# Kernel optimization log

Measured on AMD Instinct MI355X. Metric: run time of the kernel, lower is better.

Reference implementation:

```python
import jax, jax.numpy as jnp
import numpy as np

B, N, C, H = 4, 1024, 1024, 16
DH = C // H  # 64
EPS = 1e-5   # nn.LayerNorm default


def _layernorm(x, g, b):
    m = x.mean(-1, keepdims=True)
    v = ((x - m) ** 2).mean(-1, keepdims=True)
    return (x - m) * jax.lax.rsqrt(v + EPS) * g + b


def _rot_half(x):
    d = x.shape[-1] // 2
    return jnp.concatenate([-x[..., d:], x[..., :d]], axis=-1)


def _apply_rope_cat(x, emb):
    # emb: [N, 2*DH] = sin || cos (torch tensor_split(2, -1) order)
    sin, cos = jnp.split(emb, 2, axis=-1)  # each [N, DH]
    return x * cos + _rot_half(x) * sin


def setup_inputs() -> dict:
    key = jax.random.key(0)
    ks = jax.random.split(key, 12)
    s = 0.02
    x = jax.random.normal(ks[0], (B, N, C), jnp.float32)
    delta_t_emb = jax.random.normal(ks[1], (B, N, C), jnp.float32)
    v_residual_v1 = jax.random.normal(ks[2], (B, H, N, DH), jnp.float32)
    # realistic rope table: sin||cos, each DH wide (freqs repeated twice for rotate_half)
    pos = jnp.arange(N, dtype=jnp.float32)
    inv_freq = 1.0 / (10000.0 ** (jnp.arange(0, DH // 2, dtype=jnp.float32) / (DH // 2)))
    freqs = pos[:, None] * inv_freq[None, :]          # [N, DH/2]
    freqs = jnp.concatenate([freqs, freqs], axis=-1)  # [N, DH]
    rope = jnp.concatenate([jnp.sin(freqs), jnp.cos(freqs)], axis=-1)  # [N, 2*DH]
    Wqkv = jax.random.normal(ks[3], (3 * C, C), jnp.float32) * s
    bqkv = jnp.zeros((3 * C,), jnp.float32)
    Wdt = jax.random.normal(ks[4], (3 * C, C), jnp.float32) * s
    bdt = jnp.zeros((3 * C,), jnp.float32)
    qn_g = jnp.ones((DH,), jnp.float32); qn_b = jnp.zeros((DH,), jnp.float32)
    kn_g = jnp.ones((DH,), jnp.float32); kn_b = jnp.zeros((DH,), jnp.float32)
    lamb1 = jnp.asarray(0.5, jnp.float32)
    lamb2 = jnp.asarray(0.5, jnp.float32)
    Wproj = jax.random.normal(ks[5], (C, C), jnp.float32) * s
    bproj = jnp.zeros((C,), jnp.float32)
    return {
        "x": x, "rope": rope, "delta_t_emb": delta_t_emb, "v_residual_v1": v_residual_v1,
        "Wqkv": Wqkv, "bqkv": bqkv, "Wdt": Wdt, "bdt": bdt,
        "qn_g": qn_g, "qn_b": qn_b, "kn_g": kn_g, "kn_b": kn_b,
        "lamb1": lamb1, "lamb2": lamb2, "Wproj": Wproj, "bproj": bproj,
    }


def reference(x, rope, delta_t_emb, v_residual_v1, Wqkv, bqkv, Wdt, bdt,
              qn_g, qn_b, kn_g, kn_b, lamb1, lamb2, Wproj, bproj):
    b, n, c = x.shape
    # fused QKV: [B,N,3C] -> [3,B,H,N,DH]
    qkv = (jnp.einsum('bnc,oc->bno', x, Wqkv) + bqkv).reshape(b, n, 3, H, DH)
    qkv = jnp.transpose(qkv, (2, 0, 3, 1, 4))
    q, k, v = qkv[0], qkv[1], qkv[2]
    # delta-t additive embeddings
    dqkv = (jnp.einsum('bnc,oc->bno', delta_t_emb, Wdt) + bdt).reshape(b, n, 3, H, DH)
    dqkv = jnp.transpose(dqkv, (2, 0, 3, 1, 4))
    q = q + dqkv[0]; k = k + dqkv[1]; v = v + dqkv[2]
    # value-residual mixing
    v = lamb1 * v + lamb2 * v_residual_v1
    # qk layernorm over head_dim
    q = _layernorm(q, qn_g, qn_b)
    k = _layernorm(k, kn_g, kn_b)
    # RoPE (num_prefix_tokens = 0, rotate_half=True)
    q = _apply_rope_cat(q, rope)
    k = _apply_rope_cat(k, rope)
    # SDPA, non-causal, no dropout
    scale = 1.0 / jnp.sqrt(jnp.asarray(DH, x.dtype))
    scores = jnp.einsum('bhqd,bhkd->bhqk', q, k) * scale
    attn = jax.nn.softmax(scores, axis=-1)
    out = jnp.einsum('bhqk,bhkd->bhqd', attn, v)
    # [B,H,N,DH] -> [B,N,C], output norm is Identity (scale_norm=False)
    out = jnp.transpose(out, (0, 2, 1, 3)).reshape(b, n, c)
    out = jnp.einsum('bnc,oc->bno', out, Wproj) + bproj
    return out
```

## Files before the change

kernel.cpp:

```cpp
#include <hip/hip_runtime.h>
#include <stdint.h>

typedef unsigned short u16;
typedef __attribute__((ext_vector_type(8))) short short8;
typedef __attribute__((ext_vector_type(4))) float f32x4;
typedef __attribute__((ext_vector_type(4))) unsigned short u16x4;

#define DEVI __device__ __forceinline__

DEVI u16 f2bf(float f) {
  uint32_t u = __builtin_bit_cast(uint32_t, f);
  u += 0x7fffu + ((u >> 16) & 1u);
  return (u16)(u >> 16);
}

DEVI void gload_lds16(const void* g, void* l) {
  __builtin_amdgcn_global_load_lds(
      (const __attribute__((address_space(1))) void*)g,
      (__attribute__((address_space(3))) void*)(uint32_t)(uintptr_t)l,
      16, 0, 0);
}

__global__ void cvt_cat_bf16(const float* __restrict__ a, const float* __restrict__ b,
                             u16* __restrict__ dst, long total) {
  for (long i = ((long)blockIdx.x * 256 + threadIdx.x) * 4; i < total;
       i += (long)gridDim.x * 1024) {
    const long row = i >> 11;
    const long c = i & 2047;
    const float* src = (c < 1024) ? (a + row * 1024 + c) : (b + row * 1024 + (c - 1024));
    const float4 v = *(const float4*)src;
    u16x4 o = {f2bf(v.x), f2bf(v.y), f2bf(v.z), f2bf(v.w)};
    *(u16x4*)(dst + i) = o;
  }
}

__global__ void cvt_bf16(const float* __restrict__ a, u16* __restrict__ dst, long total) {
  for (long i = ((long)blockIdx.x * 256 + threadIdx.x) * 4; i < total;
       i += (long)gridDim.x * 1024) {
    const float4 v = *(const float4*)(a + i);
    u16x4 o = {f2bf(v.x), f2bf(v.y), f2bf(v.z), f2bf(v.w)};
    *(u16x4*)(dst + i) = o;
  }
}

__global__ __launch_bounds__(256, 2)
void gemm_bt(const u16* __restrict__ A, const u16* __restrict__ B,
             float* __restrict__ C, const float* __restrict__ bias1,
             const float* __restrict__ bias2, int M, int N, int K) {
  __shared__ u16 As[128 * 32];
  __shared__ u16 Bs[128 * 32];
  const int t = threadIdx.x;
  const int w = t >> 6, l = t & 63;
  const int l15 = l & 15, lg = l >> 4;
  const int bm = blockIdx.x, bn = blockIdx.y;
  const int wr = (w >> 1) * 64, wc = (w & 1) * 64;
  f32x4 acc[4][4] = {};
  const int c0 = w * 64 + l;

  for (int kt = 0; kt < (K >> 5); ++kt) {
#pragma unroll
    for (int i = 0; i < 2; ++i) {
      const int c = i * 256 + c0;
      const int row = c >> 2, seg = c & 3;
      gload_lds16(A + (long)(bm * 128 + row) * K + kt * 32 + seg * 8,
                  (char*)As + w * 1024 + i * 4096);
      gload_lds16(B + (long)(bn * 128 + row) * K + kt * 32 + seg * 8,
                  (char*)Bs + w * 1024 + i * 4096);
    }
    __syncthreads();
    short8 af[4], bfr[4];
#pragma unroll
    for (int m = 0; m < 4; ++m)
      af[m] = *(const short8*)&As[(wr + m * 16 + l15) * 32 + lg * 8];
#pragma unroll
    for (int n = 0; n < 4; ++n)
      bfr[n] = *(const short8*)&Bs[(wc + n * 16 + l15) * 32 + lg * 8];
#pragma unroll
    for (int m = 0; m < 4; ++m)
#pragma unroll
      for (int n = 0; n < 4; ++n)
        acc[m][n] = __builtin_amdgcn_mfma_f32_16x16x32_bf16(af[m], bfr[n], acc[m][n], 0, 0, 0);
    __syncthreads();
  }
#pragma unroll
  for (int m = 0; m < 4; ++m) {
    const int row0 = bm * 128 + wr + m * 16 + lg * 4;
#pragma unroll
    for (int n = 0; n < 4; ++n) {
      const int col = bn * 128 + wc + n * 16 + l15;
      float bia = 0.f;
      if (bias1) bia += bias1[col];
      if (bias2) bia += bias2[col];
#pragma unroll
      for (int r = 0; r < 4; ++r)
        C[(long)(row0 + r) * N + col] = acc[m][n][r] + bia;
    }
  }
}

__global__ __launch_bounds__(512, 2)
void gemm256(const u16* __restrict__ A, const u16* __restrict__ B,
             float* __restrict__ C, const float* __restrict__ bias1,
             const float* __restrict__ bias2, int M, int N, int K) {
  __shared__ u16 lds[4][16384];
  const int t = threadIdx.x;
  const int w = t >> 6, l = t & 63;
  const int l15 = l & 15, lg = l >> 4;
  const int wr = w >> 2, wc = w & 3;
  const int nbn = N >> 8;
  const int nb = gridDim.x;
  const int bid = blockIdx.x;
  const int lid = ((nb & 7) == 0) ? ((bid & 7) * (nb >> 3) + (bid >> 3)) : bid;
  const int bm = lid / nbn, bn = lid % nbn;
  const long rowA0 = (long)bm * 256;
  const long rowB0 = (long)bn * 256;
  const int nkt = K >> 5;

  const int su = (l & 7) ^ (l >> 3);
  const int rsub = 2 * (l >> 3) + (su >> 2);
  const int sg = su & 3;
  const int sfr = (lg + 4 * (l15 & 1)) ^ (l15 >> 1);

  f32x4 acc[8][4] = {};

#define STAGE(KT)                                                              \
  {                                                                            \
    const int _b = (KT) & 3;                                                   \
    _Pragma("unroll") for (int i = 0; i < 2; ++i) {                            \
      const int r = i * 128 + w * 16 + rsub;                                   \
      gload_lds16(A + (rowA0 + r) * K + (KT) * 32 + sg * 8,                    \
                  (char*)&lds[_b][(i * 64 + w * 8) * 64]);                     \
      gload_lds16(B + (rowB0 + r) * K + (KT) * 32 + sg * 8,                    \
                  (char*)&lds[_b][8192 + (i * 64 + w * 8) * 64]);              \
    }                                                                          \
  }

#define TILE(KT, VMSTR, DO_STAGE)                                              \
  {                                                                            \
    asm volatile("s_waitcnt vmcnt(" VMSTR ")" ::: "memory");                   \
    __builtin_amdgcn_s_barrier();                                              \
    asm volatile("" ::: "memory");                                             \
    __builtin_amdgcn_sched_barrier(0);                                         \
    if (DO_STAGE) STAGE((KT) + 3);                                             \
    const u16* bufp = lds[(KT) & 3];                                           \
    short8 bfr[4];                                                             \
    _Pragma("unroll") for (int n = 0; n < 4; ++n) {                            \
      const int p = wc * 32 + n * 8 + (l15 >> 1);                              \
      bfr[n] = *(const short8*)&bufp[8192 + p * 64 + sfr * 8];                 \
    }                                                                          \
    __builtin_amdgcn_s_setprio(1);                                             \
    _Pragma("unroll") for (int m = 0; m < 8; ++m) {                            \
      const int p = wr * 64 + m * 8 + (l15 >> 1);                              \
      const short8 af = *(const short8*)&bufp[p * 64 + sfr * 8];               \
      _Pragma("unroll") for (int n = 0; n < 4; ++n)                            \
        acc[m][n] = __builtin_amdgcn_mfma_f32_16x16x32_bf16(af, bfr[n],        \
                                                            acc[m][n], 0, 0, 0); \
    }                                                                          \
    __builtin_amdgcn_s_setprio(0);                                             \
  }

  STAGE(0)
  STAGE(1)
  STAGE(2)
  for (int kt = 0; kt < nkt - 2; ++kt) TILE(kt, "8", (kt + 3 < nkt))
  TILE(nkt - 2, "4", false)
  TILE(nkt - 1, "0", false)
#undef TILE
#undef STAGE

#pragma unroll
  for (int m = 0; m < 8; ++m) {
    const int row0 = bm * 256 + wr * 128 + m * 16 + lg * 4;
#pragma unroll
    for (int n = 0; n < 4; ++n) {
      const int col = bn * 256 + wc * 64 + n * 16 + l15;
      float bia = 0.f;
      if (bias1) bia += bias1[col];
      if (bias2) bia += bias2[col];
#pragma unroll
      for (int r = 0; r < 4; ++r)
        C[(long)(row0 + r) * N + col] = acc[m][n][r] + bia;
    }
  }
}

__global__ __launch_bounds__(256)
void fuse_qkv2(const float* __restrict__ qkv, const float* __restrict__ vres,
               const float* __restrict__ rope,
               const float* __restrict__ qg, const float* __restrict__ qb,
               const float* __restrict__ kg, const float* __restrict__ kb,
               const float* __restrict__ pl1, const float* __restrict__ pl2,
               u16* __restrict__ Q, u16* __restrict__ Ksw, u16* __restrict__ VTsw) {
  __shared__ u16 Vl[64][72];
  const int t = threadIdx.x, w = t >> 6, d = t & 63;
  const int bh = blockIdx.x, ntile = blockIdx.y;
  const int b = bh >> 4, h = bh & 15, n0 = ntile * 64;
  const float l1 = pl1[0], l2 = pl2[0];
  const float gq = qg[d], bq = qb[d];
  const float gk = kg[d], bk = kb[d];
  const float sgn = (d < 32) ? -1.f : 1.f;
  const int c = d >> 3, d7 = d & 7;

  for (int i = 0; i < 16; ++i) {
    const int nl = w * 16 + i;
    const int n = n0 + nl;
    const long base = ((long)(b * 1024 + n)) * 3072 + h * 64 + d;
    float q = qkv[base];
    float k = qkv[base + 1024];
    float v = qkv[base + 2048];
    v = l1 * v + l2 * vres[((long)(bh * 1024 + n)) * 64 + d];
    const float sinv = rope[n * 128 + d];
    const float cosv = rope[n * 128 + 64 + d];
    float s = q;
#pragma unroll
    for (int off = 1; off < 64; off <<= 1) s += __shfl_xor(s, off);
    const float qc = q - s * (1.f / 64.f);
    float vs = qc * qc;
#pragma unroll
    for (int off = 1; off < 64; off <<= 1) vs += __shfl_xor(vs, off);
    const float qn = qc * (1.f / sqrtf(vs * (1.f / 64.f) + 1e-5f)) * gq + bq;
    float s2 = k;
#pragma unroll
    for (int off = 1; off < 64; off <<= 1) s2 += __shfl_xor(s2, off);
    const float kc = k - s2 * (1.f / 64.f);
    float vs2 = kc * kc;
#pragma unroll
    for (int off = 1; off < 64; off <<= 1) vs2 += __shfl_xor(vs2, off);
    const float kn = kc * (1.f / sqrtf(vs2 * (1.f / 64.f) + 1e-5f)) * gk + bk;
    const float qo = __shfl_xor(qn, 32);
    const float ko = __shfl_xor(kn, 32);
    const float qr = qn * cosv + sgn * qo * sinv;
    const float kr = kn * cosv + sgn * ko * sinv;
    Q[(long)bh * 65536 + (long)n * 64 + d] = f2bf(qr);
    Ksw[(long)bh * 65536 + (long)n * 64 + ((c ^ (n & 7)) * 8 + d7)] = f2bf(kr);
    Vl[nl][d] = f2bf(v);
  }
  __syncthreads();
#pragma unroll
  for (int i = 0; i < 2; ++i) {
    const int task = i * 256 + t;
    const int dd = task >> 3, cc = task & 7;
    short8 o;
#pragma unroll
    for (int u = 0; u < 8; ++u) o[u] = (short)Vl[cc * 8 + u][dd];
    *(short8*)&VTsw[((long)(bh * 64 + dd)) * 1024 + n0 + ((cc ^ (dd & 7)) * 8)] = o;
  }
}

__global__ __launch_bounds__(256, 4)
void attn_fwd2(const u16* __restrict__ Q, const u16* __restrict__ Ksw,
               const u16* __restrict__ VTsw, u16* __restrict__ Out) {
  __shared__ u16 Kl[64 * 64];
  __shared__ u16 Vl[64 * 64];
  __shared__ u16 Pl[4][16 * 64];
  const int t = threadIdx.x, w = t >> 6, l = t & 63;
  const int l15 = l & 15, lg = l >> 4;
  const int x7 = l15 & 7;
  const int bh = blockIdx.x, q0 = blockIdx.y * 64;
  const long bo = (long)bh * 65536;
  u16* Plw = &Pl[w][0];

  const int qrow = q0 + w * 16 + l15;
  short8 qf[2];
#pragma unroll
  for (int ks = 0; ks < 2; ++ks)
    qf[ks] = *(const short8*)&Q[bo + (long)qrow * 64 + ks * 32 + lg * 8];

  f32x4 acc[4] = {};
  float m_run = -1e30f, l_run = 0.f;

  for (int kv = 0; kv < 16; ++kv) {
    const int kvb = kv * 64;
#pragma unroll
    for (int i = 0; i < 2; ++i) {
      const int idx = i * 256 + t;
      const int row = idx >> 3, seg = idx & 7;
      gload_lds16(Ksw + bo + (long)(kvb + row) * 64 + seg * 8, (char*)Kl + idx * 16);
      gload_lds16(VTsw + bo + (long)row * 1024 + kvb + seg * 8, (char*)Vl + idx * 16);
    }
    __syncthreads();
    f32x4 p[4];
#pragma unroll
    for (int mt = 0; mt < 4; ++mt) {
      f32x4 ps = {};
#pragma unroll
      for (int ks = 0; ks < 2; ++ks) {
        const short8 kf =
            *(const short8*)&Kl[(mt * 16 + l15) * 64 + (((ks * 4 + lg) ^ x7) * 8)];
        ps = __builtin_amdgcn_mfma_f32_16x16x32_bf16(kf, qf[ks], ps, 0, 0, 0);
      }
      p[mt] = ps;
    }
    float mx = p[0][0];
#pragma unroll
    for (int mt = 0; mt < 4; ++mt)
#pragma unroll
      for (int r = 0; r < 4; ++r) mx = fmaxf(mx, p[mt][r]);
    mx = fmaxf(mx, __shfl_xor(mx, 16));
    mx = fmaxf(mx, __shfl_xor(mx, 32));
    const float mnew = fmaxf(m_run, mx * 0.125f);
    const float alpha = __expf(m_run - mnew);
    m_run = mnew;
    float sum = 0.f;
#pragma unroll
    for (int mt = 0; mt < 4; ++mt)
#pragma unroll
      for (int r = 0; r < 4; ++r) {
        const float e = __expf(p[mt][r] * 0.125f - mnew);
        p[mt][r] = e;
        sum += e;
      }
    sum += __shfl_xor(sum, 16);
    sum += __shfl_xor(sum, 32);
    l_run = l_run * alpha + sum;
#pragma unroll
    for (int mt = 0; mt < 4; ++mt) {
      const int c = mt * 2 + (lg >> 1);
      char* bp = (char*)Plw + l15 * 128 + ((c ^ x7) * 16) + (lg & 1) * 8;
      *(uint32_t*)bp = (uint32_t)f2bf(p[mt][0]) | ((uint32_t)f2bf(p[mt][1]) << 16);
      *(uint32_t*)(bp + 4) = (uint32_t)f2bf(p[mt][2]) | ((uint32_t)f2bf(p[mt][3]) << 16);
    }
#pragma unroll
    for (int mt = 0; mt < 4; ++mt)
#pragma unroll
      for (int r = 0; r < 4; ++r) acc[mt][r] *= alpha;
#pragma unroll
    for (int ks = 0; ks < 2; ++ks) {
      const short8 pf =
          *(const short8*)((char*)Plw + l15 * 128 + (((ks * 4 + lg) ^ x7) * 16));
#pragma unroll
      for (int mt = 0; mt < 4; ++mt) {
        const short8 vf =
            *(const short8*)&Vl[(mt * 16 + l15) * 64 + (((ks * 4 + lg) ^ x7) * 8)];
        acc[mt] = __builtin_amdgcn_mfma_f32_16x16x32_bf16(vf, pf, acc[mt], 0, 0, 0);
      }
    }
    __syncthreads();
  }
  const int b = bh >> 4, h = bh & 15;
  const float inv = 1.f / l_run;
  const long obase = ((long)(b * 1024 + qrow)) * 1024 + h * 64;
#pragma unroll
  for (int mt = 0; mt < 4; ++mt) {
    const long o = obase + mt * 16 + lg * 4;
    *(uint32_t*)&Out[o] =
        (uint32_t)f2bf(acc[mt][0] * inv) | ((uint32_t)f2bf(acc[mt][1] * inv) << 16);
    *(uint32_t*)&Out[o + 2] =
        (uint32_t)f2bf(acc[mt][2] * inv) | ((uint32_t)f2bf(acc[mt][3] * inv) << 16);
  }
}

extern "C" void kernel_launch(void* const* d_in, const int* in_sizes, int n_in,
                              void* d_out, int out_size, void* d_ws, size_t ws_size,
                              hipStream_t stream) {
  const float* x     = (const float*)d_in[0];
  const float* rope  = (const float*)d_in[1];
  const float* dte   = (const float*)d_in[2];
  const float* vres  = (const float*)d_in[3];
  const float* Wqkv  = (const float*)d_in[4];
  const float* bqkv  = (const float*)d_in[5];
  const float* Wdt   = (const float*)d_in[6];
  const float* bdt   = (const float*)d_in[7];
  const float* qn_g  = (const float*)d_in[8];
  const float* qn_b  = (const float*)d_in[9];
  const float* kn_g  = (const float*)d_in[10];
  const float* kn_b  = (const float*)d_in[11];
  const float* l1    = (const float*)d_in[12];
  const float* l2    = (const float*)d_in[13];
  const float* Wproj = (const float*)d_in[14];
  const float* bproj = (const float*)d_in[15];
  float* out = (float*)d_out;

  char* ws = (char*)d_ws;
  u16*   A_cat = (u16*)(ws);
  u16*   W_cat = (u16*)(ws + 16777216);
  u16*   Wp    = (u16*)(ws + 29360128);
  float* qkv   = (float*)(ws + 31457280);
  u16*   Qb    = (u16*)(ws + 81788928);
  u16*   Ksw   = (u16*)(ws + 90177536);
  u16*   VTsw  = (u16*)(ws + 98566144);
  u16*   AO    = (u16*)(ws + 106954752);

  cvt_cat_bf16<<<2048, 256, 0, stream>>>(x, dte, A_cat, (long)4096 * 2048);
  cvt_cat_bf16<<<2048, 256, 0, stream>>>(Wqkv, Wdt, W_cat, (long)3072 * 2048);
  cvt_bf16<<<1024, 256, 0, stream>>>(Wproj, Wp, (long)1024 * 1024);
  gemm256<<<192, 512, 0, stream>>>(A_cat, W_cat, qkv, bqkv, bdt, 4096, 3072, 2048);
  fuse_qkv2<<<dim3(64, 16), 256, 0, stream>>>(qkv, vres, rope, qn_g, qn_b, kn_g, kn_b,
                                              l1, l2, Qb, Ksw, VTsw);
  attn_fwd2<<<dim3(64, 16), 256, 0, stream>>>(Qb, Ksw, VTsw, AO);
  gemm_bt<<<dim3(32, 8), 256, 0, stream>>>(AO, Wp, out, bproj, nullptr, 4096, 1024, 1024);
}
```

Baseline: 173.6 us.

## Split GEMM k-tile into two half-phases interleaving LDS reads, staging, and MFMA

```diff
diff --git a/kernel.cpp b/kernel.cpp
--- a/kernel.cpp
+++ b/kernel.cpp
@@ -123,50 +123,86 @@
 
   f32x4 acc[8][4] = {};
 
-#define STAGE(KT)                                                              \
+#define STAGE_A(KT)                                                            \
   {                                                                            \
     const int _b = (KT) & 3;                                                   \
     _Pragma("unroll") for (int i = 0; i < 2; ++i) {                            \
       const int r = i * 128 + w * 16 + rsub;                                   \
       gload_lds16(A + (rowA0 + r) * K + (KT) * 32 + sg * 8,                    \
                   (char*)&lds[_b][(i * 64 + w * 8) * 64]);                     \
+    }                                                                          \
+  }
+#define STAGE_B(KT)                                                            \
+  {                                                                            \
+    const int _b = (KT) & 3;                                                   \
+    _Pragma("unroll") for (int i = 0; i < 2; ++i) {                            \
+      const int r = i * 128 + w * 16 + rsub;                                   \
       gload_lds16(B + (rowB0 + r) * K + (KT) * 32 + sg * 8,                    \
                   (char*)&lds[_b][8192 + (i * 64 + w * 8) * 64]);              \
     }                                                                          \
   }
 
-#define TILE(KT, VMSTR, DO_STAGE)                                              \
+#define TILE(KT, DO_STAGE, DO_VM, JSTR)                                        \
   {                                                                            \
-    asm volatile("s_waitcnt vmcnt(" VMSTR ")" ::: "memory");                   \
-    __builtin_amdgcn_s_barrier();                                              \
-    asm volatile("" ::: "memory");                                             \
-    __builtin_amdgcn_sched_barrier(0);                                         \
-    if (DO_STAGE) STAGE((KT) + 3);                                             \
     const u16* bufp = lds[(KT) & 3];                                           \
-    short8 bfr[4];                                                             \
+                \
+    short8 bfr[4], alo[4];                                                     \
     _Pragma("unroll") for (int n = 0; n < 4; ++n) {                            \
       const int p = wc * 32 + n * 8 + (l15 >> 1);                              \
       bfr[n] = *(const short8*)&bufp[8192 + p * 64 + sfr * 8];                 \
     }                                                                          \
+    _Pragma("unroll") for (int m = 0; m < 4; ++m) {                            \
+      const int p = wr * 64 + m * 8 + (l15 >> 1);                              \
+      alo[m] = *(const short8*)&bufp[p * 64 + sfr * 8];                        \
+    }                                                                          \
+    if (DO_STAGE) STAGE_A((KT) + 3);                                           \
+    __builtin_amdgcn_sched_barrier(0);                                         \
+    __builtin_amdgcn_s_barrier();                                              \
+    asm volatile("s_waitcnt lgkmcnt(0)" ::: "memory");                         \
+    __builtin_amdgcn_sched_barrier(0);                                         \
     __builtin_amdgcn_s_setprio(1);                                             \
-    _Pragma("unroll") for (int m = 0; m < 8; ++m) {                            \
-      const int p = wr * 64 + m * 8 + (l15 >> 1);                              \
-      const short8 af = *(const short8*)&bufp[p * 64 + sfr * 8];               \
+    _Pragma("unroll") for (int m = 0; m < 4; ++m)                              \
       _Pragma("unroll") for (int n = 0; n < 4; ++n)                            \
-        acc[m][n] = __builtin_amdgcn_mfma_f32_16x16x32_bf16(af, bfr[n],        \
+        acc[m][n] = __builtin_amdgcn_mfma_f32_16x16x32_bf16(alo[m], bfr[n],    \
                                                             acc[m][n], 0, 0, 0); \
+    __builtin_amdgcn_s_setprio(0);                                             \
+    __builtin_amdgcn_sched_barrier(0);                                         \
+    __builtin_amdgcn_s_barrier();                                              \
+         \
+    short8 ahi[4];                                                             \
+    _Pragma("unroll") for (int m = 0; m < 4; ++m) {                            \
+      const int p = wr * 64 + (m + 4) * 8 + (l15 >> 1);                        \
+      ahi[m] = *(const short8*)&bufp[p * 64 + sfr * 8];                        \
     }                                                                          \
+    if (DO_STAGE) STAGE_B((KT) + 3);                                           \
+    __builtin_amdgcn_sched_barrier(0);                                         \
+    __builtin_amdgcn_s_barrier();                                              \
+    asm volatile("s_waitcnt lgkmcnt(0)" ::: "memory");                         \
+    __builtin_amdgcn_sched_barrier(0);                                         \
+    __builtin_amdgcn_s_setprio(1);                                             \
+    _Pragma("unroll") for (int m = 0; m < 4; ++m)                              \
+      _Pragma("unroll") for (int n = 0; n < 4; ++n)                            \
+        acc[m + 4][n] = __builtin_amdgcn_mfma_f32_16x16x32_bf16(               \
+            ahi[m], bfr[n], acc[m + 4][n], 0, 0, 0);                           \
     __builtin_amdgcn_s_setprio(0);                                             \
-  }
-
-  STAGE(0)
-  STAGE(1)
-  STAGE(2)
-  for (int kt = 0; kt < nkt - 2; ++kt) TILE(kt, "8", (kt + 3 < nkt))
-  TILE(nkt - 2, "4", false)
-  TILE(nkt - 1, "0", false)
+    if (DO_VM) asm volatile("s_waitcnt vmcnt(" JSTR ")" ::: "memory");         \
+    __builtin_amdgcn_sched_barrier(0);                                         \
+    __builtin_amdgcn_s_barrier();                                              \
+  }
+
+  STAGE_A(0); STAGE_B(0);
+  STAGE_A(1); STAGE_B(1);
+  STAGE_A(2); STAGE_B(2);
+  asm volatile("s_waitcnt vmcnt(8)" ::: "memory");
+  __builtin_amdgcn_s_barrier();
+
+  for (int kt = 0; kt < nkt - 3; ++kt) TILE(kt, 1, 1, "8")
+  TILE(nkt - 3, 0, 1, "4")
+  TILE(nkt - 2, 0, 1, "0")
+  TILE(nkt - 1, 0, 0, "0")
 #undef TILE
-#undef STAGE
+#undef STAGE_A
+#undef STAGE_B
 
 #pragma unroll
   for (int m = 0; m < 8; ++m) {
```

Result: no change. 173.0 us (-0.3%).
